# Performance work log

Hardware: AMD Instinct MI355X
Metric: run time of the kernel (lower is better)

The kernel has to match this reference:

```python
import jax, jax.numpy as jnp
import numpy as np

B, N, D = 4, 2048, 512
H = 8
HD = D // H
MLP_H = 4 * D
SCALE = HD ** -0.5
ELEV_SCALE = 1000.0
EPS = 1e-5


def _ln(x, g, b):
    m = jnp.mean(x, axis=-1, keepdims=True)
    v = jnp.mean((x - m) ** 2, axis=-1, keepdims=True)
    return (x - m) * jax.lax.rsqrt(v + EPS) * g + b


def setup_inputs() -> dict:
    key = jax.random.key(0)
    ks = jax.random.split(key, 10)
    s = lambda fin: (2.0 / fin) ** 0.5
    return {
        "x": jax.random.normal(ks[0], (B, N, D), jnp.float32),
        "elevation_patches": jax.random.uniform(ks[1], (B, N), jnp.float32) * 3000.0,
        "ln1_g": jnp.ones((D,), jnp.float32),
        "ln1_b": jnp.zeros((D,), jnp.float32),
        "qkv_w": jax.random.normal(ks[2], (D, 3 * D), jnp.float32) * s(D),
        "alpha": jnp.ones((1,), jnp.float32),
        "proj_w": jax.random.normal(ks[3], (D, D), jnp.float32) * s(D),
        "proj_b": jnp.zeros((D,), jnp.float32),
        "ln2_g": jnp.ones((D,), jnp.float32),
        "ln2_b": jnp.zeros((D,), jnp.float32),
        "fc1_w": jax.random.normal(ks[4], (D, MLP_H), jnp.float32) * s(D),
        "fc1_b": jnp.zeros((MLP_H,), jnp.float32),
        "fc2_w": jax.random.normal(ks[5], (MLP_H, D), jnp.float32) * s(MLP_H),
        "fc2_b": jnp.zeros((D,), jnp.float32),
    }


def reference(x, elevation_patches, ln1_g, ln1_b, qkv_w, alpha, proj_w, proj_b,
              ln2_g, ln2_b, fc1_w, fc1_b, fc2_w, fc2_b):
    # --- attention ---
    h = _ln(x, ln1_g, ln1_b)
    qkv = (h @ qkv_w).reshape(B, N, 3, H, HD)
    q, k, v = (jnp.moveaxis(qkv[:, :, i], 1, 2) for i in range(3))  # [B,H,N,HD]
    scores = jnp.einsum('bhnd,bhmd->bhnm', q, k) * SCALE
    elev_diff = (elevation_patches[:, None, :] - elevation_patches[:, :, None]) / ELEV_SCALE
    bias = jnp.clip(-alpha[0] * jax.nn.relu(elev_diff), -10.0, 0.0)  # [B,N,N]
    attn = jax.nn.softmax(scores + bias[:, None], axis=-1)
    out = jnp.einsum('bhnm,bhmd->bhnd', attn, v)
    out = jnp.moveaxis(out, 1, 2).reshape(B, N, D) @ proj_w + proj_b
    x = x + out
    # --- mlp ---
    h2 = _ln(x, ln2_g, ln2_b)
    mlp = jax.nn.gelu(h2 @ fc1_w + fc1_b, approximate=False) @ fc2_w + fc2_b
    return x + mlp
```

## Files before the change

kernel.cpp:

```cpp
#include <hip/hip_runtime.h>
#include <math.h>

typedef unsigned short u16;
typedef unsigned int u32;

#define B_ 4
#define N_ 2048
#define D_ 512
#define H_ 8
#define HD_ 64
#define MLP_H_ 2048
#define EPS_ 1e-5f
#define C2_ 14.426950408889634f
#define QSCALE_ 0.1803368801111204f
#define EL2_ 0.0014426950408889634f

#if __has_builtin(__builtin_amdgcn_exp2f)
#define EXP2(x) __builtin_amdgcn_exp2f(x)
#else
#define EXP2(x) exp2f(x)
#endif

__device__ __forceinline__ u16 bf16_rne(float x) {
  u32 u = __float_as_uint(x);
  u32 r = (u + 0x7FFFu + ((u >> 16) & 1u)) >> 16;
  return (u16)r;
}
#if __has_builtin(__builtin_amdgcn_cvt_pk_bf16_f32)
typedef __bf16 bf2_t __attribute__((ext_vector_type(2)));
__device__ __forceinline__ u32 pk_bf16(float a, float b) {
  bf2_t v = __builtin_amdgcn_cvt_pk_bf16_f32(a, b);
  u32 r; __builtin_memcpy(&r, &v, 4); return r;
}
#else
__device__ __forceinline__ u32 pk_bf16(float a, float b) {
  return (u32)bf16_rne(a) | ((u32)bf16_rne(b) << 16);
}
#endif
__device__ __forceinline__ void bf16_split(float x, u16& h, u16& l) {
  h = bf16_rne(x);
  float hf = __uint_as_float(((u32)h) << 16);
  l = bf16_rne(x - hf);
}

typedef __attribute__((ext_vector_type(8))) short bfrag;
typedef __attribute__((ext_vector_type(4))) float ffrag;

#define LDS_AS(p) ((__attribute__((address_space(3))) void*)(p))
#define GLB_AS(p) ((const __attribute__((address_space(1))) void*)(p))

__global__ __launch_bounds__(256) void ln_kernel(
    const float* __restrict__ x, const float* __restrict__ g,
    const float* __restrict__ b, u16* __restrict__ o,
    const float* __restrict__ elev, const float* __restrict__ alpha,
    float* __restrict__ e2)
{
  __shared__ float red[8];
  int row = blockIdx.x;
  int tid = threadIdx.x;
  if (e2 && tid == 0) e2[row] = elev[row] * (alpha[0] * EL2_);
  const float* xr = x + (size_t)row * D_;
  float v0 = xr[tid], v1 = xr[tid + 256];
  float s = v0 + v1;
  #pragma unroll
  for (int off = 32; off > 0; off >>= 1) s += __shfl_xor(s, off, 64);
  if ((tid & 63) == 0) red[tid >> 6] = s;
  __syncthreads();
  float mean = (red[0] + red[1] + red[2] + red[3]) * (1.0f / D_);
  float d0 = v0 - mean, d1 = v1 - mean;
  float vs = d0 * d0 + d1 * d1;
  #pragma unroll
  for (int off = 32; off > 0; off >>= 1) vs += __shfl_xor(vs, off, 64);
  if ((tid & 63) == 0) red[4 + (tid >> 6)] = vs;
  __syncthreads();
  float var = (red[4] + red[5] + red[6] + red[7]) * (1.0f / D_);
  float r = rsqrtf(var + EPS_);
  u16* orow = o + (size_t)row * D_;
  orow[tid]       = bf16_rne(d0 * r * g[tid] + b[tid]);
  orow[tid + 256] = bf16_rne(d1 * r * g[tid + 256] + b[tid + 256]);
}

__device__ __forceinline__ void wsplit_body(
    const float* __restrict__ W, u16* __restrict__ Thi, u16* __restrict__ Tlo,
    int K, int N, int bx, int by, int tid)
{
  __shared__ float tile[64][65];
  int n0 = bx * 64, k0 = by * 64;
  int c = tid & 63, r4 = tid >> 6;
  #pragma unroll
  for (int i = 0; i < 16; i++) {
    int r = r4 + i * 4;
    tile[r][c] = W[(size_t)(k0 + r) * N + n0 + c];
  }
  __syncthreads();
  #pragma unroll
  for (int i = 0; i < 16; i++) {
    int rn = r4 + i * 4;
    float v = tile[c][rn];
    size_t o = (size_t)(n0 + rn) * K + k0 + c;
    if (Tlo) {
      u16 h, l; bf16_split(v, h, l);
      Thi[o] = h; Tlo[o] = l;
    } else {
      Thi[o] = bf16_rne(v);
    }
  }
}

__global__ __launch_bounds__(256) void wsplit_all(
    const float* __restrict__ qkv_w, const float* __restrict__ proj_w,
    const float* __restrict__ fc1_w, const float* __restrict__ fc2_w,
    u16* __restrict__ qw_hi, u16* __restrict__ qw_lo,
    u16* __restrict__ pw_hi, u16* __restrict__ f1_hi, u16* __restrict__ f2_hi)
{
  int id = blockIdx.x;
  int tid = threadIdx.x;
  if (id < 192) {
    wsplit_body(qkv_w, qw_hi, qw_lo, 512, 1536, id % 24, id / 24, tid);
  } else if (id < 256) {
    int l = id - 192;
    wsplit_body(proj_w, pw_hi, nullptr, 512, 512, l % 8, l / 8, tid);
  } else if (id < 512) {
    int l = id - 256;
    wsplit_body(fc1_w, f1_hi, nullptr, 512, 2048, l % 32, l / 32, tid);
  } else {
    int l = id - 512;
    wsplit_body(fc2_w, f2_hi, nullptr, 2048, 512, l % 8, l / 8, tid);
  }
}

template<int ROWS>
__device__ __forceinline__ void stage32(const u16* __restrict__ src, int ld,
                                        int r0, int k0, u16* lds, int lane, int wave)
{
  #pragma unroll
  for (int i = 0; i < ROWS / 64; i++) {
    int seg = wave * (ROWS / 64) + i;
    int chunk = seg * 64 + lane;
    int r = chunk >> 2;
    int c = (chunk & 3) ^ ((r >> 1) & 3);
    const u16* g = src + (size_t)(r0 + r) * ld + k0 + c * 8;
    __builtin_amdgcn_global_load_lds(GLB_AS(g), LDS_AS((char*)lds + seg * 1024), 16, 0, 0);
  }
}

__device__ __forceinline__ int swz_off(int R, int quad) {
  return R * 32 + ((quad ^ ((R >> 1) & 3)) * 8);
}

template<int TBM, int TBN, int WR, int WC, int TERMS, int VT>
__global__ __launch_bounds__(256) void gemm_tpl(
    const u16* __restrict__ Ahi,
    const u16* __restrict__ Whi, const u16* __restrict__ Wlo,
    const float* __restrict__ bias, const float* __restrict__ res,
    float* __restrict__ Cf, u16* __restrict__ Ohi, u16* __restrict__ Olo,
    int M, int K, int N, int act, int qcols)
{
  constexpr int MF = TBM / (WR * 16);
  constexpr int NF = TBN / (WC * 16);
  constexpr int AT = TBM * 32;
  constexpr int BT = TBN * 32;
  constexpr int SMEMU = 2 * AT + ((TERMS >= 2) ? 4 * BT : 2 * BT);
  __shared__ __align__(16) u16 smem[SMEMU];
  u16* As0 = smem;               u16* As1 = smem + AT;
  u16* Bh0 = smem + 2 * AT;      u16* Bh1 = smem + 2 * AT + BT;
  u16* Bl0 = smem + 2 * AT + 2 * BT;
  u16* Bl1 = smem + 2 * AT + 3 * BT;

  int tid = threadIdx.x;
  int lane = tid & 63, wave = tid >> 6;
  int wr = wave / WC, wc = wave % WC;
  int ln = lane & 15, quad = lane >> 4;
  int m0 = blockIdx.y * TBM, n0 = blockIdx.x * TBN;

  ffrag acc[MF][NF] = {};

  for (int k0 = 0; k0 < K; k0 += 64) {
    stage32<TBM>(Ahi, K, m0, k0,      As0, lane, wave);
    stage32<TBM>(Ahi, K, m0, k0 + 32, As1, lane, wave);
    stage32<TBN>(Whi, K, n0, k0,      Bh0, lane, wave);
    stage32<TBN>(Whi, K, n0, k0 + 32, Bh1, lane, wave);
    if constexpr (TERMS >= 2) {
      stage32<TBN>(Wlo, K, n0, k0,      Bl0, lane, wave);
      stage32<TBN>(Wlo, K, n0, k0 + 32, Bl1, lane, wave);
    }
    __syncthreads();

    #pragma unroll
    for (int hf = 0; hf < 2; hf++) {
      const u16* Asf = hf ? As1 : As0;
      const u16* Bhf = hf ? Bh1 : Bh0;
      const u16* Blf = hf ? Bl1 : Bl0;
      bfrag ah[MF], bh[NF], bl[NF];
      #pragma unroll
      for (int t = 0; t < MF; t++)
        ah[t] = *(const bfrag*)(Asf + swz_off(wr * (TBM / WR) + t * 16 + ln, quad));
      #pragma unroll
      for (int u = 0; u < NF; u++) {
        int off = swz_off(wc * (TBN / WC) + u * 16 + ln, quad);
        bh[u] = *(const bfrag*)(Bhf + off);
        if constexpr (TERMS >= 2) bl[u] = *(const bfrag*)(Blf + off);
      }
      #pragma unroll
      for (int ti = 0; ti < MF; ti++) {
        #pragma unroll
        for (int tj = 0; tj < NF; tj++) {
          acc[ti][tj] = __builtin_amdgcn_mfma_f32_16x16x32_bf16(ah[ti], bh[tj], acc[ti][tj], 0, 0, 0);
          if constexpr (TERMS >= 2)
            acc[ti][tj] = __builtin_amdgcn_mfma_f32_16x16x32_bf16(ah[ti], bl[tj], acc[ti][tj], 0, 0, 0);
        }
      }
    }
    __syncthreads();
  }

  if constexpr (VT) {
    #pragma unroll
    for (int tj = 0; tj < NF; tj++) {
      int col = n0 + wc * (TBN / WC) + tj * 16 + ln;
      int h = col >> 6, d = col & 63;
      #pragma unroll
      for (int ti = 0; ti < MF; ti++) {
        int rw = m0 + wr * (TBM / WR) + ti * 16 + quad * 4;
        int bb = rw >> 11, n = rw & (N_ - 1);
        u32 w0 = pk_bf16(acc[ti][tj][0], acc[ti][tj][1]);
        u32 w1 = pk_bf16(acc[ti][tj][2], acc[ti][tj][3]);
        size_t dst = ((size_t)((bb * H_ + h) * HD_ + d)) * N_ + n;
        *(uint2*)(Ohi + dst) = make_uint2(w0, w1);
      }
    }
    return;
  }

  #pragma unroll
  for (int tj = 0; tj < NF; tj++) {
    int col = n0 + wc * (TBN / WC) + tj * 16 + ln;
    float bv = bias ? bias[col] : 0.f;
    float cs = (col < qcols) ? QSCALE_ : 1.0f;
    bool store_lo = (col < qcols);
    #pragma unroll
    for (int ti = 0; ti < MF; ti++) {
      int rw = m0 + wr * (TBM / WR) + ti * 16 + quad * 4;
      #pragma unroll
      for (int r = 0; r < 4; r++) {
        float y = acc[ti][tj][r] + bv;
        if (act) y = 0.5f * y * (1.f + erff(y * 0.70710678118654752f));
        if (res) y += res[(size_t)(rw + r) * N + col];
        if (Cf) Cf[(size_t)(rw + r) * N + col] = y;
        if (Ohi) {
          y *= cs;
          if (Olo && store_lo) {
            u16 hh, ll; bf16_split(y, hh, ll);
            Ohi[(size_t)(rw + r) * N + col] = hh;
            Olo[(size_t)(rw + r) * N + col] = ll;
          } else {
            Ohi[(size_t)(rw + r) * N + col] = bf16_rne(y);
          }
        }
      }
    }
  }
}

__device__ __forceinline__ void stage_tile64(const u16* __restrict__ gbase, size_t rstride,
                                             u16* lds, int wave, int lane)
{
  #pragma unroll
  for (int i = 0; i < 2; i++) {
    int seg = wave * 2 + i;
    int chunk = seg * 64 + lane;
    int ch = chunk >> 8;
    int pc = chunk & 255;
    int r = pc >> 2;
    int q = (pc & 3) ^ ((r >> 1) & 3);
    const u16* g = gbase + (size_t)r * rstride + ch * 32 + q * 8;
    __builtin_amdgcn_global_load_lds(GLB_AS(g), LDS_AS((char*)lds + seg * 1024), 16, 0, 0);
  }
}

__device__ __forceinline__ int frag_off(int c, int R, int quad) {
  return c * 2048 + R * 32 + ((quad ^ ((R >> 1) & 3)) * 8);
}

__global__ __launch_bounds__(256) void attn_mfma_kernel(
    const u16* __restrict__ qkh, const u16* __restrict__ qkl,
    const u16* __restrict__ vth,
    const float* __restrict__ e2, u16* __restrict__ outb)
{
  __shared__ __align__(16) u16 Kh[4096];
  __shared__ __align__(16) u16 Vh[4096];
  __shared__ __align__(16) u16 Pw[4][16][72];

  int b = blockIdx.z, h = blockIdx.y;
  int q0 = blockIdx.x * 64;
  int tid = threadIdx.x;
  int lane = tid & 63, wq = tid >> 6;
  int ln = lane & 15, quad = lane >> 4;

  const u16* qb_h = qkh + ((size_t)(b * N_ + q0)) * 1024 + h * 64;
  const u16* qb_l = qkl + ((size_t)(b * N_ + q0)) * 1024 + h * 64;
  stage_tile64(qb_h, 1024, Kh, wq, lane);
  stage_tile64(qb_l, 1024, Vh, wq, lane);
  __syncthreads();

  bfrag qfh[2], qfl[2];
  #pragma unroll
  for (int c = 0; c < 2; c++) {
    int off = frag_off(c, wq * 16 + ln, quad);
    qfh[c] = *(const bfrag*)(Kh + off);
    qfl[c] = *(const bfrag*)(Vh + off);
  }
  __syncthreads();

  float e2q = e2[b * N_ + q0 + wq * 16 + ln];
  float m_i = -3.0e38f, l_i = 0.f;
  ffrag O[4] = {};

  const u16* kp = qkh + (size_t)b * N_ * 1024 + 512 + h * 64;
  const u16* vp = vth + (size_t)(b * H_ + h) * HD_ * N_;
  const float* ep = e2 + b * N_;

  for (int k0 = 0; k0 < N_; k0 += 64) {
    stage_tile64(kp, 1024, Kh, wq, lane);
    stage_tile64(vp, N_, Vh, wq, lane);
    kp += (size_t)64 * 1024;
    vp += 64;
    __syncthreads();

    ffrag S[4];
    #pragma unroll
    for (int kt = 0; kt < 4; kt++) {
      ffrag s = {0.f, 0.f, 0.f, 0.f};
      #pragma unroll
      for (int c = 0; c < 2; c++) {
        bfrag kf = *(const bfrag*)(Kh + frag_off(c, kt * 16 + ln, quad));
        s = __builtin_amdgcn_mfma_f32_16x16x32_bf16(kf, qfh[c], s, 0, 0, 0);
        s = __builtin_amdgcn_mfma_f32_16x16x32_bf16(kf, qfl[c], s, 0, 0, 0);
      }
      S[kt] = s;
    }

    float4 ek[4];
    #pragma unroll
    for (int kt = 0; kt < 4; kt++)
      ek[kt] = *(const float4*)&ep[k0 + kt * 16 + quad * 4];

    float p[4][4];
    float mx = -3.0e38f;
    #pragma unroll
    for (int kt = 0; kt < 4; kt++) {
      #pragma unroll
      for (int r = 0; r < 4; r++) {
        float d = (&ek[kt].x)[r] - e2q;
        d = fminf(fmaxf(d, 0.f), C2_);
        float sv = S[kt][r] - d;
        p[kt][r] = sv;
        mx = fmaxf(mx, sv);
      }
    }
    mx = fmaxf(mx, __shfl_xor(mx, 16, 64));
    mx = fmaxf(mx, __shfl_xor(mx, 32, 64));
    float mnew = fmaxf(m_i, mx);
    float corr = EXP2(m_i - mnew);
    float ps = 0.f;
    #pragma unroll
    for (int kt = 0; kt < 4; kt++) {
      #pragma unroll
      for (int r = 0; r < 4; r++) {
        float pv = EXP2(p[kt][r] - mnew);
        p[kt][r] = pv;
        ps += pv;
      }
    }
    ps += __shfl_xor(ps, 16, 64);
    ps += __shfl_xor(ps, 32, 64);
    m_i = mnew;
    l_i = l_i * corr + ps;
    #pragma unroll
    for (int dt = 0; dt < 4; dt++) O[dt] *= corr;

    #pragma unroll
    for (int kt = 0; kt < 4; kt++) {
      u32 w0 = pk_bf16(p[kt][0], p[kt][1]);
      u32 w1 = pk_bf16(p[kt][2], p[kt][3]);
      *(uint2*)&Pw[wq][ln][kt * 16 + quad * 4] = make_uint2(w0, w1);
    }

    bfrag pf[2];
    #pragma unroll
    for (int c = 0; c < 2; c++)
      pf[c] = *(const bfrag*)&Pw[wq][ln][c * 32 + quad * 8];

    #pragma unroll
    for (int dt = 0; dt < 4; dt++) {
      ffrag o = O[dt];
      #pragma unroll
      for (int c = 0; c < 2; c++) {
        bfrag vf = *(const bfrag*)(Vh + frag_off(c, dt * 16 + ln, quad));
        o = __builtin_amdgcn_mfma_f32_16x16x32_bf16(vf, pf[c], o, 0, 0, 0);
      }
      O[dt] = o;
    }
    __syncthreads();
  }

  float inv = 1.0f / l_i;
  int row = q0 + wq * 16 + ln;
  #pragma unroll
  for (int dt = 0; dt < 4; dt++) {
    u32 w0 = pk_bf16(O[dt][0] * inv, O[dt][1] * inv);
    u32 w1 = pk_bf16(O[dt][2] * inv, O[dt][3] * inv);
    *(uint2*)&outb[((size_t)(b * N_ + row)) * D_ + h * 64 + dt * 16 + quad * 4] =
        make_uint2(w0, w1);
  }
}

extern "C" void kernel_launch(void* const* d_in, const int* in_sizes, int n_in,
                              void* d_out, int out_size, void* d_ws, size_t ws_size,
                              hipStream_t stream) {
  const float* x      = (const float*)d_in[0];
  const float* elev   = (const float*)d_in[1];
  const float* ln1_g  = (const float*)d_in[2];
  const float* ln1_b  = (const float*)d_in[3];
  const float* qkv_w  = (const float*)d_in[4];
  const float* alpha  = (const float*)d_in[5];
  const float* proj_w = (const float*)d_in[6];
  const float* proj_b = (const float*)d_in[7];
  const float* ln2_g  = (const float*)d_in[8];
  const float* ln2_b  = (const float*)d_in[9];
  const float* fc1_w  = (const float*)d_in[10];
  const float* fc1_b  = (const float*)d_in[11];
  const float* fc2_w  = (const float*)d_in[12];
  const float* fc2_b  = (const float*)d_in[13];
  float* out = (float*)d_out;

  const size_t HBf  = (size_t)B_ * N_ * D_;
  const size_t QKE  = (size_t)B_ * N_ * 1024;
  const size_t MLPE = (size_t)B_ * N_ * MLP_H_;

  char* p = (char*)d_ws;
  u16* abuf = (u16*)p;                     p += HBf * 2;
  char* region = p;                        p += MLPE * 2;
  u16* qkh    = (u16*)region;
  u16* qkl    = (u16*)(region + QKE * 2);
  u16* mlp_hi = (u16*)region;
  u16* vth  = (u16*)p;  p += HBf * 2;
  float* xres = (float*)p;                 p += HBf * 4;
  u16* qw_hi = (u16*)p;  p += (size_t)D_ * 3 * D_ * 2;
  u16* qw_lo = (u16*)p;  p += (size_t)D_ * 3 * D_ * 2;
  u16* pw_hi = (u16*)p;  p += (size_t)D_ * D_ * 2;
  u16* f1_hi = (u16*)p;  p += (size_t)D_ * MLP_H_ * 2;
  u16* f2_hi = (u16*)p;  p += (size_t)MLP_H_ * D_ * 2;
  float* e2  = (float*)p; p += (size_t)B_ * N_ * 4;

  const int rows = B_ * N_;

  wsplit_all<<<768, 256, 0, stream>>>(qkv_w, proj_w, fc1_w, fc2_w,
                                      qw_hi, qw_lo, pw_hi, f1_hi, f2_hi);
  ln_kernel<<<rows, 256, 0, stream>>>(x, ln1_g, ln1_b, abuf, elev, alpha, e2);
  gemm_tpl<128, 64, 4, 1, 2, 0><<<dim3(1024 / 64, rows / 128), 256, 0, stream>>>(
      abuf, qw_hi, qw_lo, nullptr, nullptr,
      nullptr, qkh, qkl, rows, D_, 1024, 0, D_);
  gemm_tpl<64, 64, 2, 2, 1, 1><<<dim3(512 / 64, rows / 64), 256, 0, stream>>>(
      abuf, qw_hi + (size_t)1024 * D_, nullptr, nullptr, nullptr,
      nullptr, vth, nullptr, rows, D_, 512, 0, 0);
  attn_mfma_kernel<<<dim3(N_ / 64, H_, B_), 256, 0, stream>>>(
      qkh, qkl, vth, e2, abuf);
  gemm_tpl<64, 64, 2, 2, 1, 0><<<dim3(D_ / 64, rows / 64), 256, 0, stream>>>(
      abuf, pw_hi, nullptr, proj_b, x,
      xres, nullptr, nullptr, rows, D_, D_, 0, 0);
  ln_kernel<<<rows, 256, 0, stream>>>(xres, ln2_g, ln2_b, abuf, nullptr, nullptr, nullptr);
  gemm_tpl<64, 128, 1, 4, 1, 0><<<dim3(MLP_H_ / 128, rows / 64), 256, 0, stream>>>(
      abuf, f1_hi, nullptr, fc1_b, nullptr,
      nullptr, mlp_hi, nullptr, rows, D_, MLP_H_, 1, 0);
  gemm_tpl<64, 64, 2, 2, 1, 0><<<dim3(D_ / 64, rows / 64), 256, 0, stream>>>(
      mlp_hi, f2_hi, nullptr, fc2_b, xres,
      out, nullptr, nullptr, rows, MLP_H_, D_, 0, 0);
}
```

Measured before the change: 350.9 us.

## Fuse QKV GEMMs into one kernel and double-buffer K/V tiles in attention

Measured after the change: 356.3 us. Within noise of the previous version (+1.5%).

```diff
diff --git a/kernel.cpp b/kernel.cpp
--- a/kernel.cpp
+++ b/kernel.cpp
@@ -19,6 +19,11 @@
 #define EXP2(x) __builtin_amdgcn_exp2f(x)
 #else
 #define EXP2(x) exp2f(x)
+#endif
+#if __has_builtin(__builtin_amdgcn_fmed3f)
+#define CLAMP0C(x) __builtin_amdgcn_fmed3f((x), 0.0f, C2_)
+#else
+#define CLAMP0C(x) fminf(fmaxf((x), 0.0f), C2_)
 #endif
 
 __device__ __forceinline__ u16 bf16_rne(float x) {
@@ -148,24 +153,106 @@
   return R * 32 + ((quad ^ ((R >> 1) & 3)) * 8);
 }
 
-template<int TBM, int TBN, int WR, int WC, int TERMS, int VT>
-__global__ __launch_bounds__(256) void gemm_tpl(
+__global__ __launch_bounds__(256) void qkv_gemm(
     const u16* __restrict__ Ahi,
     const u16* __restrict__ Whi, const u16* __restrict__ Wlo,
+    u16* __restrict__ qkh, u16* __restrict__ qkl, u16* __restrict__ vth)
+{
+  __shared__ __align__(16) u16 As0[128 * 32], As1[128 * 32];
+  __shared__ __align__(16) u16 Bh0[64 * 32],  Bh1[64 * 32];
+  __shared__ __align__(16) u16 Bl0[64 * 32],  Bl1[64 * 32];
+
+  int tid = threadIdx.x;
+  int lane = tid & 63, wave = tid >> 6;
+  int ln = lane & 15, quad = lane >> 4;
+  int m0 = blockIdx.y * 128, n0 = blockIdx.x * 64;
+  bool lo = (n0 < 1024);
+
+  ffrag acc[2][4] = {};
+
+  for (int k0 = 0; k0 < D_; k0 += 64) {
+    stage32<128>(Ahi, D_, m0, k0,      As0, lane, wave);
+    stage32<128>(Ahi, D_, m0, k0 + 32, As1, lane, wave);
+    stage32<64>(Whi, D_, n0, k0,      Bh0, lane, wave);
+    stage32<64>(Whi, D_, n0, k0 + 32, Bh1, lane, wave);
+    if (lo) {
+      stage32<64>(Wlo, D_, n0, k0,      Bl0, lane, wave);
+      stage32<64>(Wlo, D_, n0, k0 + 32, Bl1, lane, wave);
+    }
+    __syncthreads();
+
+    #pragma unroll
+    for (int hf = 0; hf < 2; hf++) {
+      const u16* Asf = hf ? As1 : As0;
+      const u16* Bhf = hf ? Bh1 : Bh0;
+      const u16* Blf = hf ? Bl1 : Bl0;
+      bfrag ah[2], bh[4], bl[4];
+      #pragma unroll
+      for (int t = 0; t < 2; t++)
+        ah[t] = *(const bfrag*)(Asf + swz_off(wave * 32 + t * 16 + ln, quad));
+      #pragma unroll
+      for (int u = 0; u < 4; u++) {
+        int off = swz_off(u * 16 + ln, quad);
+        bh[u] = *(const bfrag*)(Bhf + off);
+        bl[u] = *(const bfrag*)(Blf + off);
+      }
+      #pragma unroll
+      for (int ti = 0; ti < 2; ti++) {
+        #pragma unroll
+        for (int tj = 0; tj < 4; tj++) {
+          acc[ti][tj] = __builtin_amdgcn_mfma_f32_16x16x32_bf16(ah[ti], bh[tj], acc[ti][tj], 0, 0, 0);
+          if (lo)
+            acc[ti][tj] = __builtin_amdgcn_mfma_f32_16x16x32_bf16(ah[ti], bl[tj], acc[ti][tj], 0, 0, 0);
+        }
+      }
+    }
+    __syncthreads();
+  }
+
+  #pragma unroll
+  for (int tj = 0; tj < 4; tj++) {
+    int col = n0 + tj * 16 + ln;
+    #pragma unroll
+    for (int ti = 0; ti < 2; ti++) {
+      int rw = m0 + wave * 32 + ti * 16 + quad * 4;
+      if (col < 512) {
+        #pragma unroll
+        for (int r = 0; r < 4; r++) {
+          float y = acc[ti][tj][r] * QSCALE_;
+          u16 hh, ll; bf16_split(y, hh, ll);
+          qkh[(size_t)(rw + r) * 1024 + col] = hh;
+          qkl[(size_t)(rw + r) * 1024 + col] = ll;
+        }
+      } else if (col < 1024) {
+        #pragma unroll
+        for (int r = 0; r < 4; r++)
+          qkh[(size_t)(rw + r) * 1024 + col] = bf16_rne(acc[ti][tj][r]);
+      } else {
+        int h = (col - 1024) >> 6, d = (col - 1024) & 63;
+        int bb = rw >> 11, n = rw & (N_ - 1);
+        u32 w0 = pk_bf16(acc[ti][tj][0], acc[ti][tj][1]);
+        u32 w1 = pk_bf16(acc[ti][tj][2], acc[ti][tj][3]);
+        size_t dst = ((size_t)((bb * H_ + h) * HD_ + d)) * N_ + n;
+        *(uint2*)(vth + dst) = make_uint2(w0, w1);
+      }
+    }
+  }
+}
+
+template<int TBM, int TBN, int WR, int WC>
+__global__ __launch_bounds__(256) void gemm_tpl(
+    const u16* __restrict__ Ahi, const u16* __restrict__ Whi,
     const float* __restrict__ bias, const float* __restrict__ res,
-    float* __restrict__ Cf, u16* __restrict__ Ohi, u16* __restrict__ Olo,
-    int M, int K, int N, int act, int qcols)
+    float* __restrict__ Cf, u16* __restrict__ Ohi,
+    int M, int K, int N, int act)
 {
   constexpr int MF = TBM / (WR * 16);
   constexpr int NF = TBN / (WC * 16);
   constexpr int AT = TBM * 32;
   constexpr int BT = TBN * 32;
-  constexpr int SMEMU = 2 * AT + ((TERMS >= 2) ? 4 * BT : 2 * BT);
-  __shared__ __align__(16) u16 smem[SMEMU];
-  u16* As0 = smem;               u16* As1 = smem + AT;
-  u16* Bh0 = smem + 2 * AT;      u16* Bh1 = smem + 2 * AT + BT;
-  u16* Bl0 = smem + 2 * AT + 2 * BT;
-  u16* Bl1 = smem + 2 * AT + 3 * BT;
+  __shared__ __align__(16) u16 smem[2 * AT + 2 * BT];
+  u16* As0 = smem;          u16* As1 = smem + AT;
+  u16* Bh0 = smem + 2 * AT; u16* Bh1 = smem + 2 * AT + BT;
 
   int tid = threadIdx.x;
   int lane = tid & 63, wave = tid >> 6;
@@ -180,64 +267,32 @@
     stage32<TBM>(Ahi, K, m0, k0 + 32, As1, lane, wave);
     stage32<TBN>(Whi, K, n0, k0,      Bh0, lane, wave);
     stage32<TBN>(Whi, K, n0, k0 + 32, Bh1, lane, wave);
-    if constexpr (TERMS >= 2) {
-      stage32<TBN>(Wlo, K, n0, k0,      Bl0, lane, wave);
-      stage32<TBN>(Wlo, K, n0, k0 + 32, Bl1, lane, wave);
-    }
     __syncthreads();
 
     #pragma unroll
     for (int hf = 0; hf < 2; hf++) {
       const u16* Asf = hf ? As1 : As0;
       const u16* Bhf = hf ? Bh1 : Bh0;
-      const u16* Blf = hf ? Bl1 : Bl0;
-      bfrag ah[MF], bh[NF], bl[NF];
+      bfrag ah[MF], bh[NF];
       #pragma unroll
       for (int t = 0; t < MF; t++)
         ah[t] = *(const bfrag*)(Asf + swz_off(wr * (TBM / WR) + t * 16 + ln, quad));
       #pragma unroll
-      for (int u = 0; u < NF; u++) {
-        int off = swz_off(wc * (TBN / WC) + u * 16 + ln, quad);
-        bh[u] = *(const bfrag*)(Bhf + off);
-        if constexpr (TERMS >= 2) bl[u] = *(const bfrag*)(Blf + off);
-      }
-      #pragma unroll
-      for (int ti = 0; ti < MF; ti++) {
+      for (int u = 0; u < NF; u++)
+        bh[u] = *(const bfrag*)(Bhf + swz_off(wc * (TBN / WC) + u * 16 + ln, quad));
+      #pragma unroll
+      for (int ti = 0; ti < MF; ti++)
         #pragma unroll
-        for (int tj = 0; tj < NF; tj++) {
+        for (int tj = 0; tj < NF; tj++)
           acc[ti][tj] = __builtin_amdgcn_mfma_f32_16x16x32_bf16(ah[ti], bh[tj], acc[ti][tj], 0, 0, 0);
-          if constexpr (TERMS >= 2)
-            acc[ti][tj] = __builtin_amdgcn_mfma_f32_16x16x32_bf16(ah[ti], bl[tj], acc[ti][tj], 0, 0, 0);
-        }
-      }
     }
     __syncthreads();
-  }
-
-  if constexpr (VT) {
-    #pragma unroll
-    for (int tj = 0; tj < NF; tj++) {
-      int col = n0 + wc * (TBN / WC) + tj * 16 + ln;
-      int h = col >> 6, d = col & 63;
-      #pragma unroll
-      for (int ti = 0; ti < MF; ti++) {
-        int rw = m0 + wr * (TBM / WR) + ti * 16 + quad * 4;
-        int bb = rw >> 11, n = rw & (N_ - 1);
-        u32 w0 = pk_bf16(acc[ti][tj][0], acc[ti][tj][1]);
-        u32 w1 = pk_bf16(acc[ti][tj][2], acc[ti][tj][3]);
-        size_t dst = ((size_t)((bb * H_ + h) * HD_ + d)) * N_ + n;
-        *(uint2*)(Ohi + dst) = make_uint2(w0, w1);
-      }
-    }
-    return;
   }
 
   #pragma unroll
   for (int tj = 0; tj < NF; tj++) {
     int col = n0 + wc * (TBN / WC) + tj * 16 + ln;
     float bv = bias ? bias[col] : 0.f;
-    float cs = (col < qcols) ? QSCALE_ : 1.0f;
-    bool store_lo = (col < qcols);
     #pragma unroll
     for (int ti = 0; ti < MF; ti++) {
       int rw = m0 + wr * (TBM / WR) + ti * 16 + quad * 4;
@@ -247,16 +302,7 @@
         if (act) y = 0.5f * y * (1.f + erff(y * 0.70710678118654752f));
         if (res) y += res[(size_t)(rw + r) * N + col];
         if (Cf) Cf[(size_t)(rw + r) * N + col] = y;
-        if (Ohi) {
-          y *= cs;
-          if (Olo && store_lo) {
-            u16 hh, ll; bf16_split(y, hh, ll);
-            Ohi[(size_t)(rw + r) * N + col] = hh;
-            Olo[(size_t)(rw + r) * N + col] = ll;
-          } else {
-            Ohi[(size_t)(rw + r) * N + col] = bf16_rne(y);
-          }
-        }
+        if (Ohi) Ohi[(size_t)(rw + r) * N + col] = bf16_rne(y);
       }
     }
   }
@@ -287,8 +333,8 @@
     const u16* __restrict__ vth,
     const float* __restrict__ e2, u16* __restrict__ outb)
 {
-  __shared__ __align__(16) u16 Kh[4096];
-  __shared__ __align__(16) u16 Vh[4096];
+  __shared__ __align__(16) u16 Kh[2][4096];
+  __shared__ __align__(16) u16 Vh[2][4096];
   __shared__ __align__(16) u16 Pw[4][16][72];
 
   int b = blockIdx.z, h = blockIdx.y;
@@ -299,16 +345,16 @@
 
   const u16* qb_h = qkh + ((size_t)(b * N_ + q0)) * 1024 + h * 64;
   const u16* qb_l = qkl + ((size_t)(b * N_ + q0)) * 1024 + h * 64;
-  stage_tile64(qb_h, 1024, Kh, wq, lane);
-  stage_tile64(qb_l, 1024, Vh, wq, lane);
+  stage_tile64(qb_h, 1024, Kh[0], wq, lane);
+  stage_tile64(qb_l, 1024, Vh[0], wq, lane);
   __syncthreads();
 
   bfrag qfh[2], qfl[2];
   #pragma unroll
   for (int c = 0; c < 2; c++) {
     int off = frag_off(c, wq * 16 + ln, quad);
-    qfh[c] = *(const bfrag*)(Kh + off);
-    qfl[c] = *(const bfrag*)(Vh + off);
+    qfh[c] = *(const bfrag*)(Kh[0] + off);
+    qfl[c] = *(const bfrag*)(Vh[0] + off);
   }
   __syncthreads();
 
@@ -320,12 +366,20 @@
   const u16* vp = vth + (size_t)(b * H_ + h) * HD_ * N_;
   const float* ep = e2 + b * N_;
 
-  for (int k0 = 0; k0 < N_; k0 += 64) {
-    stage_tile64(kp, 1024, Kh, wq, lane);
-    stage_tile64(vp, N_, Vh, wq, lane);
-    kp += (size_t)64 * 1024;
-    vp += 64;
-    __syncthreads();
+  stage_tile64(kp, 1024, Kh[0], wq, lane);
+  stage_tile64(vp, N_, Vh[0], wq, lane);
+  kp += (size_t)64 * 1024;
+  vp += 64;
+  __syncthreads();
+
+  for (int it = 0; it < N_ / 64; it++) {
+    int cur = it & 1;
+    if (it < N_ / 64 - 1) {
+      stage_tile64(kp, 1024, Kh[cur ^ 1], wq, lane);
+      stage_tile64(vp, N_, Vh[cur ^ 1], wq, lane);
+      kp += (size_t)64 * 1024;
+      vp += 64;
+    }
 
     ffrag S[4];
     #pragma unroll
@@ -333,7 +387,7 @@
       ffrag s = {0.f, 0.f, 0.f, 0.f};
       #pragma unroll
       for (int c = 0; c < 2; c++) {
-        bfrag kf = *(const bfrag*)(Kh + frag_off(c, kt * 16 + ln, quad));
+        bfrag kf = *(const bfrag*)(Kh[cur] + frag_off(c, kt * 16 + ln, quad));
         s = __builtin_amdgcn_mfma_f32_16x16x32_bf16(kf, qfh[c], s, 0, 0, 0);
         s = __builtin_amdgcn_mfma_f32_16x16x32_bf16(kf, qfl[c], s, 0, 0, 0);
       }
@@ -343,7 +397,7 @@
     float4 ek[4];
     #pragma unroll
     for (int kt = 0; kt < 4; kt++)
-      ek[kt] = *(const float4*)&ep[k0 + kt * 16 + quad * 4];
+      ek[kt] = *(const float4*)&ep[it * 64 + kt * 16 + quad * 4];
 
     float p[4][4];
     float mx = -3.0e38f;
@@ -351,8 +405,7 @@
     for (int kt = 0; kt < 4; kt++) {
       #pragma unroll
       for (int r = 0; r < 4; r++) {
-        float d = (&ek[kt].x)[r] - e2q;
-        d = fminf(fmaxf(d, 0.f), C2_);
+        float d = CLAMP0C((&ek[kt].x)[r] - e2q);
         float sv = S[kt][r] - d;
         p[kt][r] = sv;
         mx = fmaxf(mx, sv);
@@ -396,7 +449,7 @@
       ffrag o = O[dt];
       #pragma unroll
       for (int c = 0; c < 2; c++) {
-        bfrag vf = *(const bfrag*)(Vh + frag_off(c, dt * 16 + ln, quad));
+        bfrag vf = *(const bfrag*)(Vh[cur] + frag_off(c, dt * 16 + ln, quad));
         o = __builtin_amdgcn_mfma_f32_16x16x32_bf16(vf, pf[c], o, 0, 0, 0);
       }
       O[dt] = o;
@@ -458,22 +511,15 @@
   wsplit_all<<<768, 256, 0, stream>>>(qkv_w, proj_w, fc1_w, fc2_w,
                                       qw_hi, qw_lo, pw_hi, f1_hi, f2_hi);
   ln_kernel<<<rows, 256, 0, stream>>>(x, ln1_g, ln1_b, abuf, elev, alpha, e2);
-  gemm_tpl<128, 64, 4, 1, 2, 0><<<dim3(1024 / 64, rows / 128), 256, 0, stream>>>(
-      abuf, qw_hi, qw_lo, nullptr, nullptr,
-      nullptr, qkh, qkl, rows, D_, 1024, 0, D_);
-  gemm_tpl<64, 64, 2, 2, 1, 1><<<dim3(512 / 64, rows / 64), 256, 0, stream>>>(
-      abuf, qw_hi + (size_t)1024 * D_, nullptr, nullptr, nullptr,
-      nullptr, vth, nullptr, rows, D_, 512, 0, 0);
+  qkv_gemm<<<dim3(1536 / 64, rows / 128), 256, 0, stream>>>(
+      abuf, qw_hi, qw_lo, qkh, qkl, vth);
   attn_mfma_kernel<<<dim3(N_ / 64, H_, B_), 256, 0, stream>>>(
       qkh, qkl, vth, e2, abuf);
-  gemm_tpl<64, 64, 2, 2, 1, 0><<<dim3(D_ / 64, rows / 64), 256, 0, stream>>>(
-      abuf, pw_hi, nullptr, proj_b, x,
-      xres, nullptr, nullptr, rows, D_, D_, 0, 0);
+  gemm_tpl<64, 64, 2, 2><<<dim3(D_ / 64, rows / 64), 256, 0, stream>>>(
+      abuf, pw_hi, proj_b, x, xres, nullptr, rows, D_, D_, 0);
   ln_kernel<<<rows, 256, 0, stream>>>(xres, ln2_g, ln2_b, abuf, nullptr, nullptr, nullptr);
-  gemm_tpl<64, 128, 1, 4, 1, 0><<<dim3(MLP_H_ / 128, rows / 64), 256, 0, stream>>>(
-      abuf, f1_hi, nullptr, fc1_b, nullptr,
-      nullptr, mlp_hi, nullptr, rows, D_, MLP_H_, 1, 0);
-  gemm_tpl<64, 64, 2, 2, 1, 0><<<dim3(D_ / 64, rows / 64), 256, 0, stream>>>(
-      mlp_hi, f2_hi, nullptr, fc2_b, xres,
-      out, nullptr, nullptr, rows, MLP_H_, D_, 0, 0);
-}
+  gemm_tpl<64, 128, 1, 4><<<dim3(MLP_H_ / 128, rows / 64), 256, 0, stream>>>(
+      abuf, f1_hi, fc1_b, nullptr, nullptr, mlp_hi, rows, D_, MLP_H_, 1);
+  gemm_tpl<64, 64, 2, 2><<<dim3(D_ / 64, rows / 64), 256, 0, stream>>>(
+      mlp_hi, f2_hi, fc2_b, xres, out, nullptr, rows, MLP_H_, D_, 0);
+}
```
